# Kernel optimization log

Measured on AMD Instinct MI355X. Metric: run time of the kernel, lower is better.

Reference implementation:

```python
import jax, jax.numpy as jnp
import numpy as np
from jax import lax

NUM_CLASSES = 10
NUM_ITER = 3
CAP_DIM = 8       # primary capsule dim
OUT_CAP_DIM = 16  # digit capsule dim
NUM_MAP = 32      # 256 / 8
NUM_PRIM = 144    # 12*12


def squash(x, axis=-1):
    s2 = jnp.sum(x * x, axis=axis, keepdims=True)
    return (s2 / (1.0 + s2)) * x / jnp.sqrt(s2 + 1e-8)


def conv2d(x, w, b):
    y = lax.conv_general_dilated(x, w, (1, 1), 'VALID',
                                 dimension_numbers=('NCHW', 'OIHW', 'NCHW'))
    return y + b[None, :, None, None]


def setup_inputs() -> dict:
    key = jax.random.key(0)
    ks = jax.random.split(key, 13)
    B = 128
    return {
        'imgs': jax.random.uniform(ks[0], (B, 1, 28, 28), dtype=jnp.float32),
        'conv1_w': jax.random.normal(ks[1], (256, 1, 9, 9), jnp.float32) * 0.05,
        'conv1_b': jnp.zeros((256,), jnp.float32),
        'conv2_w': jax.random.normal(ks[2], (256, 256, 9, 9), jnp.float32) * 0.02,
        'conv2_b': jnp.zeros((256,), jnp.float32),
        # non-shared routing weights: [num_prim_map, num_prim_cap, num_classes, out_dim, in_dim]
        'W_digit': jax.random.normal(ks[3], (NUM_MAP, NUM_PRIM, NUM_CLASSES, OUT_CAP_DIM, CAP_DIM), jnp.float32),
        'dec_w1': jax.random.normal(ks[4], (OUT_CAP_DIM * NUM_CLASSES, 512), jnp.float32) * 0.05,
        'dec_b1': jnp.zeros((512,), jnp.float32),
        'dec_w2': jax.random.normal(ks[5], (512, 1024), jnp.float32) * 0.04,
        'dec_b2': jnp.zeros((1024,), jnp.float32),
        'dec_w3': jax.random.normal(ks[6], (1024, 784), jnp.float32) * 0.03,
        'dec_b3': jnp.zeros((784,), jnp.float32),
    }


def capsnet_fwd(imgs, conv1_w, conv1_b, conv2_w, conv2_b, W_digit,
                dec_w1, dec_b1, dec_w2, dec_b2, dec_w3, dec_b3):
    B = imgs.shape[0]
    # conv1 + relu: [B,256,20,20]
    x = jax.nn.relu(conv2d(imgs, conv1_w, conv1_b))
    # primary caps conv: [B,256,12,12]
    p = conv2d(x, conv2_w, conv2_b)
    # view [B, cap_dim, num_map, 12, 12] -> [B, num_map, 144, cap_dim]
    p = p.reshape(B, CAP_DIM, NUM_MAP, NUM_PRIM)
    p = jnp.transpose(p, (0, 2, 3, 1))
    u = squash(p, axis=-1)  # [B, 32, 144, 8]

    # u_hat[b,m,p,c,o] = W[m,p,c,o,i] * u[b,m,p,i]  (broadcast instead of repeat)
    u_hat = jnp.einsum('mpcoi,bmpi->bmpco', W_digit, u)
    u_hat = u_hat.reshape(B, NUM_MAP * NUM_PRIM, NUM_CLASSES, OUT_CAP_DIM)  # [B,4608,10,16]

    # dynamic routing
    b_ij = jnp.zeros((B, NUM_MAP * NUM_PRIM, NUM_CLASSES), u_hat.dtype)
    v = None
    for i in range(NUM_ITER):
        c_ij = jax.nn.softmax(b_ij, axis=1)                     # over input capsules
        s_j = jnp.einsum('bnc,bncd->bcd', c_ij, u_hat)          # [B,10,16]
        v = squash(s_j, axis=-1)
        if i != NUM_ITER - 1:
            b_ij = b_ij + jnp.einsum('bncd,bcd->bnc', u_hat, v)  # agreement

    # v: [B,10,16]
    v_length = jnp.sqrt(jnp.sum(v * v, axis=-1))                 # [B,10]
    y_pred = jnp.argmax(v_length, axis=1)
    y_pred_ohe = jax.nn.one_hot(y_pred, NUM_CLASSES, dtype=jnp.int32)

    masked = (v * y_pred_ohe.astype(v.dtype)[:, :, None]).reshape(B, -1)  # [B,160]
    h = jax.nn.relu(masked @ dec_w1 + dec_b1)
    h = jax.nn.relu(h @ dec_w2 + dec_b2)
    img_reconst = jax.nn.sigmoid(h @ dec_w3 + dec_b3)            # [B,784]
    return y_pred_ohe, img_reconst, v_length


def reference(imgs, conv1_w, conv1_b, conv2_w, conv2_b, W_digit,
              dec_w1, dec_b1, dec_w2, dec_b2, dec_w3, dec_b3):
    return capsnet_fwd(imgs, conv1_w, conv1_b, conv2_w, conv2_b, W_digit,
                       dec_w1, dec_b1, dec_w2, dec_b2, dec_w3, dec_b3)
```

## Files before the change

### kernel.cpp

```cpp
#include <hip/hip_runtime.h>
#include <cstdint>
#include <cstddef>

#define BB 128
#define NMAP 32
#define NPRIM 144
#define NCAP 4608
#define NCLS 10
#define ODIM 16
#define IDIM 8

#define WS_X1H  0
#define WS_X1L  6553600
#define WS_BH   13107200
#define WS_P    18415616
#define WS_U    23134208
#define WS_V    27852800
#define WS_H1   27873280
#define WS_H2   27938816
#define WS_CLS  28069888

#define OUT_REC  1280
#define OUT_LEN  101632

typedef __attribute__((ext_vector_type(8))) short short8;
typedef __attribute__((ext_vector_type(4))) float f32x4;

static __device__ __forceinline__ ushort f2bf(float f) {
    uint u = __float_as_uint(f);
    u = (u + 0x7FFFu + ((u >> 16) & 1u)) >> 16;
    return (ushort)u;
}
static __device__ __forceinline__ float bf2f(ushort h) {
    return __uint_as_float(((uint)h) << 16);
}

static __device__ __forceinline__ void gload16(const ushort* g, ushort* l) {
    __builtin_amdgcn_global_load_lds(
        (const __attribute__((address_space(1))) void*)g,
        (__attribute__((address_space(3))) void*)l, 16, 0, 0);
}


__global__ __launch_bounds__(256) void k_conv1(const float* __restrict__ img,
                                               const float* __restrict__ w,
                                               const float* __restrict__ bias,
                                               ushort* __restrict__ x1h,
                                               ushort* __restrict__ x1l) {
    __shared__ float simg[252];
    int bi = blockIdx.x;
    int y = bi % 20;
    int b = bi / 20;
    int oc = threadIdx.x;
    if (threadIdx.x < 252)
        simg[threadIdx.x] = img[(size_t)b * 784 + y * 28 + threadIdx.x];
    __syncthreads();

    float acc[20];
    float bv = bias[oc];
#pragma unroll
    for (int x = 0; x < 20; ++x) acc[x] = bv;
    const float* wp = w + oc * 81;
#pragma unroll
    for (int kh = 0; kh < 9; ++kh) {
        float r[28];
#pragma unroll
        for (int j = 0; j < 28; ++j) r[j] = simg[kh * 28 + j];
#pragma unroll
        for (int kw = 0; kw < 9; ++kw) {
            float wv = wp[kh * 9 + kw];
#pragma unroll
            for (int x = 0; x < 20; ++x)
                acc[x] = fmaf(wv, r[x + kw], acc[x]);
        }
    }
    size_t base = ((size_t)b * 400 + y * 20) * 256 + oc;
#pragma unroll
    for (int x = 0; x < 20; ++x) {
        float v = fmaxf(acc[x], 0.f);
        ushort h = f2bf(v);
        ushort lo = f2bf(v - bf2f(h));
        x1h[base + (size_t)x * 256] = h;
        x1l[base + (size_t)x * 256] = lo;
    }
}

__global__ __launch_bounds__(256) void k_prep_w2(const float* __restrict__ w2,
                                                 ushort* __restrict__ bpk) {
    int blk = blockIdx.x;
    int icc = blk >> 5, kq = (blk >> 3) & 3, ocg = blk & 7;
    int tid = threadIdx.x;
    int ocl = tid >> 3, ic8 = tid & 7;
    int oc = ocg * 32 + ocl;
    int ic = icc * 32 + kq * 8 + ic8;
    const float* src = w2 + ((size_t)oc * 256 + ic) * 81;
    size_t dbase = (size_t)icc * 16384 + (size_t)kq * 2048 + (size_t)oc * 8 + ic8;
#pragma unroll 9
    for (int t = 0; t < 81; ++t) {
        float v = src[t];
        ushort h = f2bf(v);
        ushort lo = f2bf(v - bf2f(h));
        bpk[(size_t)t * 131072 + dbase] = h;
        bpk[(size_t)t * 131072 + dbase + 8192] = lo;
    }
}

static __device__ __forceinline__ f32x4 mfma16(short8 a, short8 b, f32x4 c) {
    return __builtin_amdgcn_mfma_f32_16x16x32_bf16(a, b, c, 0, 0, 0);
}

struct FragR { short8 ah[5], al[5], bh0, bh1, bl0, bl1; };

template<int NMF>
static __device__ __forceinline__ void pre_fragR(
    FragR& f, const ushort* A_lds, const ushort* Bb, int tn,
    const int* celloff, int bro0, int bro1) {
    int kh = tn / 9, kw = tn - kh * 9;
    int tapoff = (kh * 20 + kw) * 40;
    const ushort* Bc = Bb + (tn % 6) * 8192;
#pragma unroll
    for (int i = 0; i < NMF; ++i) {
        f.ah[i] = *(const short8*)(A_lds + tapoff + celloff[i]);
        f.al[i] = *(const short8*)(A_lds + 16000 + tapoff + celloff[i]);
    }
    f.bh0 = *(const short8*)(Bc + bro0);
    f.bh1 = *(const short8*)(Bc + bro1);
    f.bl0 = *(const short8*)(Bc + 4096 + bro0);
    f.bl1 = *(const short8*)(Bc + 4096 + bro1);
}

template<int NMF>
static __device__ __forceinline__ void mfma_fragR(f32x4 (&acc)[5][2], const FragR& f) {
#pragma unroll
    for (int i = 0; i < NMF; ++i) {
        acc[i][0] = mfma16(f.ah[i], f.bh0, acc[i][0]);
        acc[i][1] = mfma16(f.ah[i], f.bh1, acc[i][1]);
    }
#pragma unroll
    for (int i = 0; i < NMF; ++i) {
        acc[i][0] = mfma16(f.ah[i], f.bl0, acc[i][0]);
        acc[i][1] = mfma16(f.ah[i], f.bl1, acc[i][1]);
    }
#pragma unroll
    for (int i = 0; i < NMF; ++i) {
        acc[i][0] = mfma16(f.al[i], f.bh0, acc[i][0]);
        acc[i][1] = mfma16(f.al[i], f.bh1, acc[i][1]);
    }
}

static __device__ __forceinline__ void stage_tap(
    const ushort* gB0, ushort* lB0, int tn, size_t gicc) {
    if (tn <= 80) {
        size_t g = (size_t)tn * 131072 + gicc;
        ushort* d = lB0 + (tn % 6) * 8192;
        gload16(gB0 + g, d);
        gload16(gB0 + g + 512, d + 512);
    }
}

template<int MF0, int NMF>
static __device__ __forceinline__ void conv2s_epi(
    const f32x4 (&acc)[5][2], const float* __restrict__ bias,
    float* __restrict__ p, int b, int oc0, int nq, int r, int kq) {
#pragma unroll
    for (int j = 0; j < 2; ++j) {
        int oc = oc0 + (nq * 2 + j) * 16 + r;
        float bv = bias[oc];
#pragma unroll
        for (int i = 0; i < NMF; ++i) {
            int row = b * 144 + (MF0 + i) * 16 + kq * 4;
#pragma unroll
            for (int reg = 0; reg < 4; ++reg)
                p[(size_t)(row + reg) * 256 + oc] = acc[i][j][reg] + bv;
        }
    }
}

__global__ __launch_bounds__(512)
__attribute__((amdgpu_waves_per_eu(2, 2)))
void k_conv2s(
    const ushort* __restrict__ x1h, const ushort* __restrict__ x1l,
    const ushort* __restrict__ bpk,
    const float* __restrict__ bias, float* __restrict__ p) {
    __shared__ __align__(16) ushort A_lds[32000];
    __shared__ __align__(16) ushort Bb[49152];

    const int tid = threadIdx.x;
    const int lane = tid & 63;
    const int wv = tid >> 6;
    const int mh = wv >> 2;
    const int nq = wv & 3;
    const int b  = blockIdx.x >> 1;
    const int nt = blockIdx.x & 1;
    const int oc0 = nt * 128;
    const int r = lane & 15, kq = lane >> 4;
    const int MF0r = mh ? 5 : 0;

    int celloff[5];
#pragma unroll
    for (int i = 0; i < 5; ++i) {
        int lm = (MF0r + i) * 16 + r;
        celloff[i] = ((lm / 12) * 20 + (lm % 12)) * 40 + kq * 8;
    }
    const int bro0 = kq * 1024 + ((nq * 2 + 0) * 16 + r) * 8;
    const int bro1 = kq * 1024 + ((nq * 2 + 1) * 16 + r) * 8;

    const int comp_w = wv >> 2, kq_w = wv & 3;
    const ushort* gB0 = bpk + comp_w * 8192 + kq_w * 2048 + oc0 * 8 + lane * 8;
    ushort* lB0 = Bb + comp_w * 4096 + kq_w * 1024;

    f32x4 acc[5][2];
#pragma unroll
    for (int i = 0; i < 5; ++i)
#pragma unroll
        for (int j = 0; j < 2; ++j)
            acc[i][j] = (f32x4){0.f, 0.f, 0.f, 0.f};

    FragR fX, fY;

    for (int icc = 0; icc < 8; ++icc) {
        const size_t gicc = (size_t)icc * 16384;
#pragma unroll
        for (int rd = 0; rd < 7; ++rd) {
            int idx = rd * 512 + tid;
            if (idx < 3200) {
                int comp = (idx >= 1600) ? 1 : 0;
                int ci = idx - comp * 1600;
                int cell = ci >> 2, cc = ci & 3;
                const ushort* src = (comp ? x1l : x1h) +
                    ((size_t)b * 400 + cell) * 256 + icc * 32 + cc * 8;
                short8 val = *(const short8*)src;
                *(short8*)(A_lds + comp * 16000 + cell * 40 + cc * 8) = val;
            }
        }
        stage_tap(gB0, lB0, 0, gicc);
        stage_tap(gB0, lB0, 1, gicc);
        stage_tap(gB0, lB0, 2, gicc);
        stage_tap(gB0, lB0, 3, gicc);
        __syncthreads();
        if (mh == 0) {
            pre_fragR<5>(fX, A_lds, Bb, 0, celloff, bro0, bro1);
            pre_fragR<5>(fY, A_lds, Bb, 1, celloff, bro0, bro1);
        } else {
            pre_fragR<4>(fX, A_lds, Bb, 0, celloff, bro0, bro1);
            pre_fragR<4>(fY, A_lds, Bb, 1, celloff, bro0, bro1);
        }

#pragma unroll 1
        for (int ph = 0; ph < 39; ++ph) {
            const int T = ph * 2;
            stage_tap(gB0, lB0, T + 4, gicc);
            stage_tap(gB0, lB0, T + 5, gicc);
            if (mh == 0) {
                mfma_fragR<5>(acc, fX);
                mfma_fragR<5>(acc, fY);
                pre_fragR<5>(fX, A_lds, Bb, T + 2, celloff, bro0, bro1);
                pre_fragR<5>(fY, A_lds, Bb, T + 3, celloff, bro0, bro1);
            } else {
                mfma_fragR<4>(acc, fX);
                mfma_fragR<4>(acc, fY);
                pre_fragR<4>(fX, A_lds, Bb, T + 2, celloff, bro0, bro1);
                pre_fragR<4>(fY, A_lds, Bb, T + 3, celloff, bro0, bro1);
            }
            __syncthreads();
        }
        if (mh == 0) {
            mfma_fragR<5>(acc, fX);
            mfma_fragR<5>(acc, fY);
            pre_fragR<5>(fX, A_lds, Bb, 80, celloff, bro0, bro1);
            mfma_fragR<5>(acc, fX);
        } else {
            mfma_fragR<4>(acc, fX);
            mfma_fragR<4>(acc, fY);
            pre_fragR<4>(fX, A_lds, Bb, 80, celloff, bro0, bro1);
            mfma_fragR<4>(acc, fX);
        }
        __syncthreads();
    }

    if (mh == 0) conv2s_epi<0, 5>(acc, bias, p, b, oc0, nq, r, kq);
    else         conv2s_epi<5, 4>(acc, bias, p, b, oc0, nq, r, kq);
}

__global__ __launch_bounds__(256) void k_squash(const float* __restrict__ p,
                                                float* __restrict__ u) {
    __shared__ float S[2048];
    const int tid = threadIdx.x;
    const int r0 = blockIdx.x * 8;
    const int b = blockIdx.x / 18;
    const int pos0 = (blockIdx.x % 18) * 8;
#pragma unroll
    for (int k = 0; k < 8; ++k)
        S[k * 256 + tid] = p[(size_t)(r0 + k) * 256 + tid];
    __syncthreads();
    const int r = tid >> 5, m = tid & 31;
    float pv[8];
    float s2 = 0.f;
#pragma unroll
    for (int i = 0; i < 8; ++i) {
        pv[i] = S[r * 256 + i * 32 + m];
        s2 = fmaf(pv[i], pv[i], s2);
    }
    float f = (s2 / (1.f + s2)) / sqrtf(s2 + 1e-8f);
    size_t n = (size_t)b * NCAP + m * NPRIM + (pos0 + r);
    float4* up = (float4*)(u + n * 8);
    up[0] = make_float4(f * pv[0], f * pv[1], f * pv[2], f * pv[3]);
    up[1] = make_float4(f * pv[4], f * pv[5], f * pv[6], f * pv[7]);
}

__global__ __launch_bounds__(256) void k_prep_wt(const float* __restrict__ Wd,
                                                 float* __restrict__ Wtv) {
    __shared__ float S[64][129];
    int c = blockIdx.x % NCLS;
    int nt = blockIdx.x / NCLS;
    int n0 = nt * 64;
    int tid = threadIdx.x;
#pragma unroll
    for (int rep = 0; rep < 32; ++rep) {
        int idx = rep * 256 + tid;
        int nl = idx >> 7, oi = idx & 127;
        S[nl][oi] = Wd[(size_t)(n0 + nl) * 1280 + c * 128 + oi];
    }
    __syncthreads();
#pragma unroll
    for (int rep = 0; rep < 4; ++rep) {
        int idx = rep * 256 + tid;
        int o = idx >> 6, nl = idx & 63;
        float4* d4 = (float4*)(Wtv + (((size_t)c * 16 + o) * NCAP + n0 + nl) * 8);
        d4[0] = make_float4(S[nl][o * 8 + 0], S[nl][o * 8 + 1],
                            S[nl][o * 8 + 2], S[nl][o * 8 + 3]);
        d4[1] = make_float4(S[nl][o * 8 + 4], S[nl][o * 8 + 5],
                            S[nl][o * 8 + 6], S[nl][o * 8 + 7]);
    }
}

__global__ __launch_bounds__(256) void k_route5(const float* __restrict__ u,
                                                const float* __restrict__ Wtv,
                                                float* __restrict__ v_out) {
    __shared__ float part[4][2][17];
    __shared__ float sums[2][17];
    __shared__ float vsh[2][16];
    int id = blockIdx.x;
    int c, bg;
    if (id < 512) { c = id & 7; bg = id >> 3; }
    else { int rr = id - 512; c = 8 + (rr >> 6); bg = rr & 63; }
    int b0 = bg * 2;
    int tid = threadIdx.x;
    int lane = tid & 63, wvi = tid >> 6;
    const float* WtC = Wtv + (size_t)c * 16 * NCAP * 8;

    float bij[18][2];
#pragma unroll
    for (int j = 0; j < 18; ++j) { bij[j][0] = 0.f; bij[j][1] = 0.f; }

    for (int iter = 0; iter < 3; ++iter) {
        float sZ[2] = {0.f, 0.f};
        float sS[2][16];
#pragma unroll
        for (int o = 0; o < 16; ++o) { sS[0][o] = 0.f; sS[1][o] = 0.f; }

        for (int j = 0; j < 18; ++j) {
            int n = j * 256 + tid;
            const float4* up0 = (const float4*)(u + ((size_t)b0 * NCAP + n) * 8);
            const float4* up1 = (const float4*)(u + ((size_t)(b0 + 1) * NCAP + n) * 8);
            float4 a0 = up0[0], a1 = up0[1];
            float4 c0 = up1[0], c1 = up1[1];
            float u0[8] = {a0.x, a0.y, a0.z, a0.w, a1.x, a1.y, a1.z, a1.w};
            float u1[8] = {c0.x, c0.y, c0.z, c0.w, c1.x, c1.y, c1.z, c1.w};
            float uh[2][16];
#pragma unroll
            for (int o = 0; o < 16; ++o) {
                const float4* wp = (const float4*)(WtC + ((size_t)o * NCAP + n) * 8);
                float4 w0 = wp[0], w1 = wp[1];
                float w[8] = {w0.x, w0.y, w0.z, w0.w, w1.x, w1.y, w1.z, w1.w};
                float s0 = 0.f, s1 = 0.f;
#pragma unroll
                for (int i = 0; i < 8; ++i) {
                    s0 = fmaf(w[i], u0[i], s0);
                    s1 = fmaf(w[i], u1[i], s1);
                }
                uh[0][o] = s0;
                uh[1][o] = s1;
            }
#pragma unroll
            for (int bb = 0; bb < 2; ++bb) {
                float e;
                if (iter == 0) {
                    e = 1.f;
                } else {
                    float agr = 0.f;
#pragma unroll
                    for (int o = 0; o < 16; ++o) agr = fmaf(uh[bb][o], vsh[bb][o], agr);
                    bij[j][bb] += agr;
                    e = __expf(bij[j][bb]);
                }
                sZ[bb] += e;
#pragma unroll
                for (int o = 0; o < 16; ++o) sS[bb][o] = fmaf(e, uh[bb][o], sS[bb][o]);
            }
        }

#pragma unroll
        for (int bb = 0; bb < 2; ++bb) {
            float z = sZ[bb];
#pragma unroll
            for (int d = 32; d >= 1; d >>= 1) z += __shfl_xor(z, d, 64);
            if (lane == 0) part[wvi][bb][0] = z;
#pragma unroll
            for (int o = 0; o < 16; ++o) {
                float s = sS[bb][o];
#pragma unroll
                for (int d = 32; d >= 1; d >>= 1) s += __shfl_xor(s, d, 64);
                if (lane == 0) part[wvi][bb][1 + o] = s;
            }
        }
        __syncthreads();
        if (tid < 34) {
            int bb = tid / 17, k = tid % 17;
            float s = 0.f;
#pragma unroll
            for (int w4 = 0; w4 < 4; ++w4) s += part[w4][bb][k];
            sums[bb][k] = s;
        }
        __syncthreads();
        if (tid < 2) {
            float Z = sums[tid][0];
            float s[16];
            float s2 = 0.f;
#pragma unroll
            for (int o = 0; o < 16; ++o) {
                s[o] = sums[tid][1 + o] / Z;
                s2 = fmaf(s[o], s[o], s2);
            }
            float f = (s2 / (1.f + s2)) / sqrtf(s2 + 1e-8f);
#pragma unroll
            for (int o = 0; o < 16; ++o) vsh[tid][o] = f * s[o];
        }
        __syncthreads();
    }
    if (tid < 32) {
        int bb = tid >> 4, o = tid & 15;
        v_out[((size_t)(b0 + bb) * NCLS + c) * 16 + o] = vsh[bb][o];
    }
}

__global__ __launch_bounds__(64) void k_head(const float* __restrict__ v,
                                             float* __restrict__ out,
                                             int* __restrict__ cls_ws) {
    __shared__ float len2[NCLS];
    __shared__ int cls_sh;
    int b = blockIdx.x, tid = threadIdx.x;
    if (tid < NCLS) {
        float s2 = 0.f;
#pragma unroll
        for (int o = 0; o < 16; ++o) {
            float t = v[((size_t)b * NCLS + tid) * 16 + o];
            s2 = fmaf(t, t, s2);
        }
        len2[tid] = s2;
        out[OUT_LEN + b * NCLS + tid] = sqrtf(s2);
    }
    __syncthreads();
    if (tid == 0) {
        int best = 0;
        float bv = len2[0];
        for (int c2 = 1; c2 < NCLS; ++c2)
            if (len2[c2] > bv) { bv = len2[c2]; best = c2; }
        cls_sh = best;
        cls_ws[b] = best;
    }
    __syncthreads();
    if (tid < NCLS) out[b * NCLS + tid] = (tid == cls_sh) ? 1.0f : 0.0f;
}

__global__ __launch_bounds__(256) void k_dec1(const float* __restrict__ v,
                                              const int* __restrict__ cls_ws,
                                              const float* __restrict__ w1,
                                              const float* __restrict__ b1,
                                              float* __restrict__ h1) {
    int id = blockIdx.x * 256 + threadIdx.x;
    int j = id % 512, b = id / 512;
    int cls = cls_ws[b];
    const float* vp = v + ((size_t)b * NCLS + cls) * 16;
    float acc = b1[j];
#pragma unroll
    for (int o = 0; o < 16; ++o)
        acc = fmaf(vp[o], w1[(size_t)(cls * 16 + o) * 512 + j], acc);
    h1[id] = fmaxf(acc, 0.f);
}

__global__ __launch_bounds__(256) void k_dec2(const float* __restrict__ h1,
                                              const float* __restrict__ w2,
                                              const float* __restrict__ b2,
                                              float* __restrict__ h2) {
    __shared__ float hs[512];
    int bi = blockIdx.x;
    int jc = bi % 4;
    int b = bi / 4;
    int tid = threadIdx.x;
    hs[tid] = h1[b * 512 + tid];
    hs[tid + 256] = h1[b * 512 + tid + 256];
    __syncthreads();
    int j = jc * 256 + tid;
    float acc = b2[j];
#pragma unroll 8
    for (int k = 0; k < 512; ++k)
        acc = fmaf(hs[k], w2[(size_t)k * 1024 + j], acc);
    h2[b * 1024 + j] = fmaxf(acc, 0.f);
}

__global__ __launch_bounds__(256) void k_dec3(const float* __restrict__ h2,
                                              const float* __restrict__ w3,
                                              const float* __restrict__ b3,
                                              float* __restrict__ out) {
    __shared__ float hs[1024];
    int bi = blockIdx.x;
    int jc = bi % 4;
    int b = bi / 4;
    int tid = threadIdx.x;
#pragma unroll
    for (int t = 0; t < 4; ++t) hs[tid + t * 256] = h2[b * 1024 + tid + t * 256];
    __syncthreads();
    int j = jc * 256 + tid;
    if (j < 784) {
        float acc = b3[j];
#pragma unroll 8
        for (int k = 0; k < 1024; ++k)
            acc = fmaf(hs[k], w3[(size_t)k * 784 + j], acc);
        out[OUT_REC + b * 784 + j] = 1.f / (1.f + __expf(-acc));
    }
}

extern "C" void kernel_launch(void* const* d_in, const int* in_sizes, int n_in,
                              void* d_out, int out_size, void* d_ws, size_t ws_size,
                              hipStream_t stream) {
    const float* imgs = (const float*)d_in[0];
    const float* c1w  = (const float*)d_in[1];
    const float* c1b  = (const float*)d_in[2];
    const float* c2w  = (const float*)d_in[3];
    const float* c2b  = (const float*)d_in[4];
    const float* Wd   = (const float*)d_in[5];
    const float* dw1  = (const float*)d_in[6];
    const float* db1  = (const float*)d_in[7];
    const float* dw2  = (const float*)d_in[8];
    const float* db2  = (const float*)d_in[9];
    const float* dw3  = (const float*)d_in[10];
    const float* db3  = (const float*)d_in[11];

    float* out = (float*)d_out;
    float* ws  = (float*)d_ws;
    ushort* x1h = (ushort*)(ws + WS_X1H);
    ushort* x1l = (ushort*)(ws + WS_X1L);
    ushort* bpk = (ushort*)(ws + WS_BH);
    float* p    = ws + WS_P;
    float* u    = ws + WS_U;
    float* v    = ws + WS_V;
    float* h1   = ws + WS_H1;
    float* h2   = ws + WS_H2;
    int*   cls  = (int*)(ws + WS_CLS);
    float* wtv  = ws + WS_X1H;

    k_conv1<<<BB * 20, 256, 0, stream>>>(imgs, c1w, c1b, x1h, x1l);
    k_prep_w2<<<256, 256, 0, stream>>>(c2w, bpk);
    k_conv2s<<<BB * 2, 512, 0, stream>>>(x1h, x1l, bpk, c2b, p);
    k_squash<<<BB * NCAP / 256, 256, 0, stream>>>(p, u);
    k_prep_wt<<<720, 256, 0, stream>>>(Wd, wtv);
    k_route5<<<(BB / 2) * NCLS, 256, 0, stream>>>(u, wtv, v);
    k_head<<<BB, 64, 0, stream>>>(v, out, cls);
    k_dec1<<<BB * 512 / 256, 256, 0, stream>>>(v, cls, dw1, db1, h1);
    k_dec2<<<BB * 4, 256, 0, stream>>>(h1, dw2, db2, h2);
    k_dec3<<<BB * 4, 256, 0, stream>>>(h2, dw3, db3, out);
}
```

Measured before the change: 1.124 ms.

## Route four batches per block, split output dims across half-blocks, keep logits in LDS

The routing kernel now handles four batch items per block instead of two, which halves the number of times each W_digit slice is read from global memory. Within a block, the 16 output dims are split between the two halves of the threads, so each thread computes 8 dims for 128 capsules. The routing logits move from registers into shared memory, and the partial agreements from the two halves are exchanged through a double-buffered LDS array. This costs a __syncthreads per capsule tile in later iterations and roughly 80KB of LDS per block, which limits occupancy, and the grid has half as many blocks.

```diff
diff --git a/kernel.cpp b/kernel.cpp
--- a/kernel.cpp
+++ b/kernel.cpp
@@ -334,96 +334,118 @@
     }
 }
 
-__global__ __launch_bounds__(256) void k_route5(const float* __restrict__ u,
+__global__ __launch_bounds__(256) void k_route7(const float* __restrict__ u,
                                                 const float* __restrict__ Wtv,
                                                 float* __restrict__ v_out) {
-    __shared__ float part[4][2][17];
-    __shared__ float sums[2][17];
-    __shared__ float vsh[2][16];
+    __shared__ float bijL[4][36][128];
+    __shared__ float agrL[2][2][4][128];
+    __shared__ float part[4][4][9];
+    __shared__ float sums[4][17];
+    __shared__ float vsh[4][16];
     int id = blockIdx.x;
     int c, bg;
-    if (id < 512) { c = id & 7; bg = id >> 3; }
-    else { int rr = id - 512; c = 8 + (rr >> 6); bg = rr & 63; }
-    int b0 = bg * 2;
+    if (id < 256) { c = id & 7; bg = id >> 3; }
+    else { int rr = id - 256; c = 8 + (rr >> 5); bg = rr & 31; }
+    int b0 = bg * 4;
     int tid = threadIdx.x;
+    int oh = tid >> 7;
+    int nl = tid & 127;
     int lane = tid & 63, wvi = tid >> 6;
-    const float* WtC = Wtv + (size_t)c * 16 * NCAP * 8;
-
-    float bij[18][2];
-#pragma unroll
-    for (int j = 0; j < 18; ++j) { bij[j][0] = 0.f; bij[j][1] = 0.f; }
+    const float* WtC = Wtv + ((size_t)c * 16 + oh * 8) * NCAP * 8;
 
     for (int iter = 0; iter < 3; ++iter) {
-        float sZ[2] = {0.f, 0.f};
-        float sS[2][16];
-#pragma unroll
-        for (int o = 0; o < 16; ++o) { sS[0][o] = 0.f; sS[1][o] = 0.f; }
-
-        for (int j = 0; j < 18; ++j) {
-            int n = j * 256 + tid;
-            const float4* up0 = (const float4*)(u + ((size_t)b0 * NCAP + n) * 8);
-            const float4* up1 = (const float4*)(u + ((size_t)(b0 + 1) * NCAP + n) * 8);
-            float4 a0 = up0[0], a1 = up0[1];
-            float4 c0 = up1[0], c1 = up1[1];
-            float u0[8] = {a0.x, a0.y, a0.z, a0.w, a1.x, a1.y, a1.z, a1.w};
-            float u1[8] = {c0.x, c0.y, c0.z, c0.w, c1.x, c1.y, c1.z, c1.w};
-            float uh[2][16];
-#pragma unroll
-            for (int o = 0; o < 16; ++o) {
-                const float4* wp = (const float4*)(WtC + ((size_t)o * NCAP + n) * 8);
+        float sZ[4] = {0.f, 0.f, 0.f, 0.f};
+        float sS[4][8];
+#pragma unroll
+        for (int bb = 0; bb < 4; ++bb)
+#pragma unroll
+            for (int oo = 0; oo < 8; ++oo) sS[bb][oo] = 0.f;
+
+        for (int j = 0; j < 36; ++j) {
+            int n = j * 128 + nl;
+            float uv[4][8];
+#pragma unroll
+            for (int bb = 0; bb < 4; ++bb) {
+                const float4* up = (const float4*)(u + ((size_t)(b0 + bb) * NCAP + n) * 8);
+                float4 a = up[0], d = up[1];
+                uv[bb][0] = a.x; uv[bb][1] = a.y; uv[bb][2] = a.z; uv[bb][3] = a.w;
+                uv[bb][4] = d.x; uv[bb][5] = d.y; uv[bb][6] = d.z; uv[bb][7] = d.w;
+            }
+            float uh[4][8];
+#pragma unroll
+            for (int oo = 0; oo < 8; ++oo) {
+                const float4* wp = (const float4*)(WtC + ((size_t)oo * NCAP + n) * 8);
                 float4 w0 = wp[0], w1 = wp[1];
                 float w[8] = {w0.x, w0.y, w0.z, w0.w, w1.x, w1.y, w1.z, w1.w};
-                float s0 = 0.f, s1 = 0.f;
-#pragma unroll
-                for (int i = 0; i < 8; ++i) {
-                    s0 = fmaf(w[i], u0[i], s0);
-                    s1 = fmaf(w[i], u1[i], s1);
+#pragma unroll
+                for (int bb = 0; bb < 4; ++bb) {
+                    float s = 0.f;
+#pragma unroll
+                    for (int i = 0; i < 8; ++i) s = fmaf(w[i], uv[bb][i], s);
+                    uh[bb][oo] = s;
                 }
-                uh[0][o] = s0;
-                uh[1][o] = s1;
-            }
-#pragma unroll
-            for (int bb = 0; bb < 2; ++bb) {
-                float e;
-                if (iter == 0) {
-                    e = 1.f;
-                } else {
-                    float agr = 0.f;
-#pragma unroll
-                    for (int o = 0; o < 16; ++o) agr = fmaf(uh[bb][o], vsh[bb][o], agr);
-                    bij[j][bb] += agr;
-                    e = __expf(bij[j][bb]);
+            }
+            float e[4];
+            if (iter == 0) {
+                e[0] = e[1] = e[2] = e[3] = 1.f;
+            } else {
+                float* agW = &agrL[j & 1][oh][0][0];
+#pragma unroll
+                for (int bb = 0; bb < 4; ++bb) {
+                    float ag = 0.f;
+#pragma unroll
+                    for (int oo = 0; oo < 8; ++oo)
+                        ag = fmaf(uh[bb][oo], vsh[bb][oh * 8 + oo], ag);
+                    agW[bb * 128 + nl] = ag;
                 }
-                sZ[bb] += e;
-#pragma unroll
-                for (int o = 0; o < 16; ++o) sS[bb][o] = fmaf(e, uh[bb][o], sS[bb][o]);
-            }
-        }
-
-#pragma unroll
-        for (int bb = 0; bb < 2; ++bb) {
+                __syncthreads();
+                const float* ag0 = &agrL[j & 1][0][0][0];
+                const float* ag1 = &agrL[j & 1][1][0][0];
+#pragma unroll
+                for (int bb = 0; bb < 4; ++bb) {
+                    float bold = (iter == 1) ? 0.f : bijL[bb][j][nl];
+                    float bnew = bold + ag0[bb * 128 + nl] + ag1[bb * 128 + nl];
+                    if (oh == 0) bijL[bb][j][nl] = bnew;
+                    e[bb] = __expf(bnew);
+                }
+            }
+#pragma unroll
+            for (int bb = 0; bb < 4; ++bb) {
+                if (oh == 0) sZ[bb] += e[bb];
+#pragma unroll
+                for (int oo = 0; oo < 8; ++oo)
+                    sS[bb][oo] = fmaf(e[bb], uh[bb][oo], sS[bb][oo]);
+            }
+        }
+
+#pragma unroll
+        for (int bb = 0; bb < 4; ++bb) {
             float z = sZ[bb];
 #pragma unroll
             for (int d = 32; d >= 1; d >>= 1) z += __shfl_xor(z, d, 64);
             if (lane == 0) part[wvi][bb][0] = z;
 #pragma unroll
-            for (int o = 0; o < 16; ++o) {
-                float s = sS[bb][o];
+            for (int oo = 0; oo < 8; ++oo) {
+                float s = sS[bb][oo];
 #pragma unroll
                 for (int d = 32; d >= 1; d >>= 1) s += __shfl_xor(s, d, 64);
-                if (lane == 0) part[wvi][bb][1 + o] = s;
+                if (lane == 0) part[wvi][bb][1 + oo] = s;
             }
         }
         __syncthreads();
-        if (tid < 34) {
+        if (tid < 68) {
             int bb = tid / 17, k = tid % 17;
-            float s = 0.f;
-#pragma unroll
-            for (int w4 = 0; w4 < 4; ++w4) s += part[w4][bb][k];
+            float s;
+            if (k == 0) s = part[0][bb][0] + part[1][bb][0];
+            else {
+                int o = k - 1;
+                if (o < 8) s = part[0][bb][1 + o] + part[1][bb][1 + o];
+                else       s = part[2][bb][o - 7] + part[3][bb][o - 7];
+            }
             sums[bb][k] = s;
         }
         __syncthreads();
-        if (tid < 2) {
+        if (tid < 4) {
             float Z = sums[tid][0];
             float s[16];
             float s2 = 0.f;
@@ -438,7 +460,7 @@
         }
         __syncthreads();
     }
-    if (tid < 32) {
+    if (tid < 64) {
         int bb = tid >> 4, o = tid & 15;
         v_out[((size_t)(b0 + bb) * NCLS + c) * 16 + o] = vsh[bb][o];
     }
@@ -565,7 +587,7 @@
     k_conv2s<<<BB * 2, 512, 0, stream>>>(x1h, x1l, bpk, c2b, p);
     k_squash<<<BB * NCAP / 256, 256, 0, stream>>>(p, u);
     k_prep_wt<<<720, 256, 0, stream>>>(Wd, wtv);
-    k_route5<<<(BB / 2) * NCLS, 256, 0, stream>>>(u, wtv, v);
+    k_route7<<<(BB / 4) * NCLS, 256, 0, stream>>>(u, wtv, v);
     k_head<<<BB, 64, 0, stream>>>(v, out, cls);
     k_dec1<<<BB * 512 / 256, 256, 0, stream>>>(v, cls, dw1, db1, h1);
     k_dec2<<<BB * 4, 256, 0, stream>>>(h1, dw2, db2, h2);
```

New measurement: 1.111 ms. About the same (-1.1%).
